# Kernel optimization log

Hardware: AMD Instinct MI355X
Metric: run time of the kernel (lower is better)

Reference implementation:

```python
import jax, jax.numpy as jnp
import numpy as np
from jax import lax

B = 4096
E = 8
D = 9216       # model_dim = 64*12*12
H = 128        # hidden_size_per_expert
O = 10         # output_dim


def setup_inputs() -> dict:
    key = jax.random.key(0)
    ks = jax.random.split(key, 10)
    s = lambda *sh: 1.0 / np.sqrt(np.prod(sh[1:]) if len(sh) > 1 else sh[0])
    return {
        "x": jax.random.normal(ks[0], (B, 1, 28, 28), jnp.float32),
        "conv1_w": jax.random.normal(ks[1], (32, 1, 3, 3), jnp.float32) * s(32, 1, 3, 3),
        "conv1_b": jnp.zeros((32,), jnp.float32),
        "conv2_w": jax.random.normal(ks[2], (64, 32, 3, 3), jnp.float32) * s(64, 32, 3, 3),
        "conv2_b": jnp.zeros((64,), jnp.float32),
        "gate_w": jax.random.normal(ks[3], (D, E), jnp.float32) * s(D, E),
        "w1": jax.random.normal(ks[4], (E, D, H), jnp.float32) * s(E, D, H),
        "b1": jnp.zeros((E, H), jnp.float32),
        "w2": jax.random.normal(ks[5], (E, H, O), jnp.float32) * s(E, H, O),
        "b2": jnp.zeros((E, O), jnp.float32),
    }


def _conv(x, w, b):
    y = lax.conv_general_dilated(x, w, (1, 1), "VALID",
                                 dimension_numbers=("NCHW", "OIHW", "NCHW"))
    return y + b[None, :, None, None]


def _maxpool2(x):
    return lax.reduce_window(x, -jnp.inf, lax.max,
                             (1, 1, 2, 2), (1, 1, 2, 2), "VALID")


def reference(x, conv1_w, conv1_b, conv2_w, conv2_b, gate_w, w1, b1, w2, b2):
    h = jax.nn.relu(_conv(x, conv1_w, conv1_b))            # [B,32,26,26]
    h = jax.nn.relu(_conv(h, conv2_w, conv2_b))            # [B,64,24,24]
    h = _maxpool2(h)                                       # [B,64,12,12]
    h = h.reshape(h.shape[0], -1)                          # [B,D]

    # top-1 gate: softmax over expert logits, pick argmax, scale by its prob
    logits = h @ gate_w                                    # [B,E]
    gates = jax.nn.softmax(logits, axis=-1)
    idx = jnp.argmax(logits, axis=-1)                      # [B]
    scale = jnp.take_along_axis(gates, idx[:, None], axis=1)  # [B,1]

    # expert FFN (computed densely per expert, selected per token)
    he = jax.nn.relu(jnp.einsum("bd,edh->beh", h, w1) + b1)   # [B,E,H]
    oe = jnp.einsum("beh,eho->beo", he, w2) + b2              # [B,E,O]
    out = jnp.take_along_axis(oe, idx[:, None, None], axis=1)[:, 0]  # [B,O]
    out = scale * out
    return jax.nn.log_softmax(out, axis=-1)
```

## Files before the change

kernel.cpp:

```cpp
#include <hip/hip_runtime.h>
#include <math.h>

namespace {
constexpr int kB = 4096;
constexpr int kD = 9216;
constexpr int kE = 8;
constexpr int kH = 128;
constexpr int kO = 10;
constexpr int PSTR = 32;
constexpr int KSPLIT = 8;

typedef __attribute__((ext_vector_type(8))) short short8;
typedef __attribute__((ext_vector_type(4))) float f32x4;
typedef __attribute__((ext_vector_type(4))) unsigned u32x4;

__device__ inline unsigned f2bf(float f) {
  unsigned u = __float_as_uint(f);
  return (u + 0x7fffu + ((u >> 16) & 1u)) >> 16;
}
__device__ inline float bf2f(unsigned b) { return __uint_as_float(b << 16); }

__device__ inline unsigned cvtpk(float a, float b) {
  unsigned d;
  asm("v_cvt_pk_bf16_f32 %0, %1, %2" : "=v"(d) : "v"(a), "v"(b));
  return d;
}
__device__ inline void hilo_pair(float a, float b, unsigned& hp, unsigned& lp) {
  hp = cvtpk(a, b);
  float ra = a - __uint_as_float(hp << 16);
  float rb = b - __uint_as_float(hp & 0xffff0000u);
  lp = cvtpk(ra, rb);
}

__global__ __launch_bounds__(256) void prep_w1(
    const float* __restrict__ w1, ushort* __restrict__ w1ph,
    ushort* __restrict__ w1pl, const float* __restrict__ c2w,
    ushort* __restrict__ Bph, ushort* __restrict__ Bpl,
    int* __restrict__ counts) {
  if (blockIdx.x == 0) {
    if (threadIdx.x < kE) counts[threadIdx.x] = 0;
    for (int i = threadIdx.x; i < 9 * 4 * 64 * 8; i += 256) {
      int j = i & 7, lane = (i >> 3) & 63, nt = (i >> 9) & 3, tap = i >> 11;
      int n = nt * 16 + (lane & 15);
      int c1 = (lane >> 4) * 8 + j;
      float v = c2w[(n * 32 + c1) * 9 + tap];
      unsigned hb = f2bf(v);
      Bph[i] = (ushort)hb;
      Bpl[i] = (ushort)f2bf(v - bf2f(hb));
    }
  }
  int t = blockIdx.x * 256 + threadIdx.x;
  int n = t & 127;
  int rem = t >> 7;
  int k8 = rem % 1152;
  int e = rem / 1152;
  const float* src = w1 + ((size_t)e * kD + (size_t)k8 * 8) * kH + n;
  float v[8];
#pragma unroll
  for (int j = 0; j < 8; ++j) v[j] = src[(size_t)j * kH];
  u32x4 hw, lw;
#pragma unroll
  for (int j = 0; j < 4; ++j) {
    unsigned hp, lp;
    hilo_pair(v[2 * j], v[2 * j + 1], hp, lp);
    hw[j] = hp;
    lw[j] = lp;
  }
  size_t base =
      ((((size_t)e * 288 + (k8 >> 2)) * 8 + (n >> 4)) * 64 +
       (((k8 & 3) << 4) | (n & 15))) * 8;
  *(u32x4*)(w1ph + base) = hw;
  *(u32x4*)(w1pl + base) = lw;
}

__global__ __launch_bounds__(256, 2) void conv_kernel(
    const float* __restrict__ x, const float* __restrict__ c1w,
    const float* __restrict__ c1b, const float* __restrict__ b2g,
    const ushort* __restrict__ Bph, const ushort* __restrict__ Bpl,
    float* __restrict__ h) {
  __shared__ float xs[784];
  __shared__ float w1s[288];
  __shared__ float b1s[32];
  __shared__ ushort h1h[364 * PSTR];
  __shared__ ushort h1l[364 * PSTR];
  const int b = blockIdx.x, tid = threadIdx.x;
  const int lane = tid & 63, wave = tid >> 6;

  short8 Bh[9], Bl[9];
#pragma unroll
  for (int tap = 0; tap < 9; ++tap) {
    int fi = ((tap * 4 + wave) * 64 + lane) * 8;
    Bh[tap] = *(const short8*)(Bph + fi);
    Bl[tap] = *(const short8*)(Bpl + fi);
  }
  float b2v = b2g[wave * 16 + (lane & 15)];

  const float* xb = x + (size_t)b * 784;
  for (int i = tid; i < 784; i += 256) xs[i] = xb[i];
  for (int i = tid; i < 288; i += 256) w1s[i] = c1w[i];
  if (tid < 32) b1s[tid] = c1b[tid];
  __syncthreads();

  float* hb = h + (size_t)b * kD;
  for (int pass = 0; pass < 2; ++pass) {
    for (int i = tid; i < 364 * 16; i += 256) {
      int p = i >> 4, cp = (i & 15) * 2;
      int r = p / 26, col = p - r * 26;
      const float* xr = xs + (pass * 12 + r) * 28 + col;
      const float* w0 = w1s + cp * 9;
      float v0 = b1s[cp], v1 = b1s[cp + 1];
#pragma unroll
      for (int ky = 0; ky < 3; ++ky)
#pragma unroll
        for (int kx = 0; kx < 3; ++kx) {
          float xv = xr[ky * 28 + kx];
          v0 += xv * w0[ky * 3 + kx];
          v1 += xv * w0[9 + ky * 3 + kx];
        }
      v0 = fmaxf(v0, 0.f);
      v1 = fmaxf(v1, 0.f);
      unsigned hp, lp;
      hilo_pair(v0, v1, hp, lp);
      *(unsigned*)&h1h[p * PSTR + cp] = hp;
      *(unsigned*)&h1l[p * PSTR + cp] = lp;
    }
    __syncthreads();
    const int m = lane & 15, kg = lane >> 4;
    for (int mt = 0; mt < 18; ++mt) {
      int cell = mt * 4 + (m >> 2), sub = m & 3;
      int cy = cell / 12, cx = cell - cy * 12;
      int yy = 2 * cy + (sub >> 1), xx = 2 * cx + (sub & 1);
      const ushort* ah = h1h + (yy * 26 + xx) * PSTR + kg * 8;
      const ushort* al = h1l + (yy * 26 + xx) * PSTR + kg * 8;
      f32x4 acc = {0.f, 0.f, 0.f, 0.f};
#pragma unroll
      for (int ky = 0; ky < 3; ++ky)
#pragma unroll
        for (int kx = 0; kx < 3; ++kx) {
          const int tap = ky * 3 + kx;
          short8 Ah = *(const short8*)(ah + (ky * 26 + kx) * PSTR);
          short8 Al = *(const short8*)(al + (ky * 26 + kx) * PSTR);
          acc = __builtin_amdgcn_mfma_f32_16x16x32_bf16(Al, Bh[tap], acc, 0, 0, 0);
          acc = __builtin_amdgcn_mfma_f32_16x16x32_bf16(Ah, Bl[tap], acc, 0, 0, 0);
          acc = __builtin_amdgcn_mfma_f32_16x16x32_bf16(Ah, Bh[tap], acc, 0, 0, 0);
        }
      int cellg = mt * 4 + kg;
      int gy = cellg / 12, gx = cellg - gy * 12;
      int orow = (pass * 6 + gy) * 12 + gx;
      float p0 = fmaxf(fmaxf(acc[0], acc[1]), fmaxf(acc[2], acc[3]));
      hb[(wave * 16 + m) * 144 + orow] = fmaxf(p0 + b2v, 0.f);
    }
    __syncthreads();
  }
}

__global__ __launch_bounds__(256) void gate_kernel(
    const float* __restrict__ h, const float* __restrict__ gw,
    int* __restrict__ idx, float* __restrict__ scale,
    int* __restrict__ counts) {
  const int b = blockIdx.x * 4 + (threadIdx.x >> 6);
  const int lane = threadIdx.x & 63;
  const float* hb = h + (size_t)b * kD;
  float acc[kE] = {0, 0, 0, 0, 0, 0, 0, 0};
  for (int i = lane; i < kD; i += 64) {
    float hv = hb[i];
    const float* g = gw + (size_t)i * kE;
#pragma unroll
    for (int e = 0; e < kE; ++e) acc[e] += hv * g[e];
  }
#pragma unroll
  for (int off = 32; off > 0; off >>= 1) {
#pragma unroll
    for (int e = 0; e < kE; ++e) acc[e] += __shfl_down(acc[e], off, 64);
  }
  if (lane == 0) {
    float m = acc[0];
    int bi = 0;
#pragma unroll
    for (int e = 1; e < kE; ++e)
      if (acc[e] > m) { m = acc[e]; bi = e; }
    float s = 0.f;
#pragma unroll
    for (int e = 0; e < kE; ++e) s += expf(acc[e] - m);
    idx[b] = bi;
    scale[b] = 1.0f / s;
    atomicAdd(&counts[bi], 1);
  }
}

__global__ __launch_bounds__(256) void scan_scatter(
    const int* __restrict__ counts, const int* __restrict__ idx,
    int* __restrict__ offsets, int* __restrict__ perm) {
  __shared__ int soff[kE + 1];
  __shared__ int cur[kE];
  if (threadIdx.x == 0) {
    int o = 0;
    for (int e = 0; e < kE; ++e) {
      soff[e] = o;
      cur[e] = o;
      o += counts[e];
    }
    soff[kE] = o;
  }
  __syncthreads();
  for (int b = threadIdx.x; b < kB; b += 256) {
    int e = idx[b];
    int pos = atomicAdd(&cur[e], 1);
    perm[pos] = b;
  }
  if (threadIdx.x <= kE) offsets[threadIdx.x] = soff[threadIdx.x];
}

__global__ __launch_bounds__(256) void expert_gemm(
    const float* __restrict__ h, const ushort* __restrict__ w1ph,
    const ushort* __restrict__ w1pl, const int* __restrict__ perm,
    const int* __restrict__ offsets, float* __restrict__ preact) {
  const int e = blockIdx.x, ks = blockIdx.y;
  const int start = offsets[e] + blockIdx.z * 64;
  const int end = offsets[e + 1];
  if (start >= end) return;
  const int M = min(64, end - start);
  __shared__ ushort Afh[4096];
  __shared__ ushort Afl[4096];
  __shared__ ushort Bsh[8192];
  __shared__ ushort Bsl[8192];
  __shared__ int rows[64];
  const int tid = threadIdx.x;
  if (tid < 64) rows[tid] = perm[start + min(tid, M - 1)];
  __syncthreads();
  const int wave = tid >> 6, lane = tid & 63;
  const int m15 = lane & 15, kg4 = lane >> 4;
  const int srow = tid >> 2, spart = tid & 3;
  const int kbase = ks * (kD / KSPLIT);
  const float* hp0 = h + (size_t)rows[srow] * kD + kbase + spart * 16;
  const int skstep = spart >> 1, skg = (spart & 1) * 2;
  const int sg = srow >> 4, sm = srow & 15;
  ushort* wh0 = &Afh[((skstep * 4 + sg) * 64 + skg * 16 + sm) * 8];
  ushort* wl0 = &Afl[((skstep * 4 + sg) * 64 + skg * 16 + sm) * 8];
  f32x4 acc[8];
#pragma unroll
  for (int j = 0; j < 8; ++j) acc[j] = {0.f, 0.f, 0.f, 0.f};

  for (int bk = 0; bk < kD / KSPLIT; bk += 64) {
#pragma unroll
    for (int c = 0; c < 2; ++c) {
      float4 v0 = *(const float4*)(hp0 + bk + c * 8);
      float4 v1 = *(const float4*)(hp0 + bk + c * 8 + 4);
      float f[8] = {v0.x, v0.y, v0.z, v0.w, v1.x, v1.y, v1.z, v1.w};
      u32x4 hw, lw;
#pragma unroll
      for (int j = 0; j < 4; ++j) {
        unsigned hp, lp;
        hilo_pair(f[2 * j], f[2 * j + 1], hp, lp);
        hw[j] = hp;
        lw[j] = lp;
      }
      *(u32x4*)(wh0 + c * 128) = hw;
      *(u32x4*)(wl0 + c * 128) = lw;
    }
    {
      const size_t bbase =
          ((size_t)e * 288 + ((kbase + bk) >> 5)) * 4096;
#pragma unroll
      for (int q = 0; q < 4; ++q) {
        int c = tid + q * 256;
        *(short8*)&Bsh[c * 8] = *(const short8*)(w1ph + bbase + (size_t)c * 8);
        *(short8*)&Bsl[c * 8] = *(const short8*)(w1pl + bbase + (size_t)c * 8);
      }
    }
    __syncthreads();
#pragma unroll
    for (int kstep = 0; kstep < 2; ++kstep) {
      const ushort* af = &Afh[((kstep * 4 + wave) * 64 + lane) * 8];
      short8 ah = *(const short8*)af;
      short8 al = *(const short8*)(af + (Afl - Afh));
      const ushort* bph = &Bsh[kstep * 4096 + lane * 8];
      const ushort* bpl = &Bsl[kstep * 4096 + lane * 8];
#pragma unroll
      for (int nt = 0; nt < 8; ++nt) {
        short8 bh = *(const short8*)(bph + nt * 512);
        short8 bl = *(const short8*)(bpl + nt * 512);
        acc[nt] = __builtin_amdgcn_mfma_f32_16x16x32_bf16(al, bh, acc[nt], 0, 0, 0);
        acc[nt] = __builtin_amdgcn_mfma_f32_16x16x32_bf16(ah, bl, acc[nt], 0, 0, 0);
        acc[nt] = __builtin_amdgcn_mfma_f32_16x16x32_bf16(ah, bh, acc[nt], 0, 0, 0);
      }
    }
    __syncthreads();
  }
  float* pb = preact + (size_t)ks * kB * kH;
#pragma unroll
  for (int r = 0; r < 4; ++r) {
    int row = wave * 16 + kg4 * 4 + r;
    if (row < M) {
      float* pr = pb + (size_t)rows[row] * kH + m15;
#pragma unroll
      for (int nt = 0; nt < 8; ++nt) pr[nt * 16] = acc[nt][r];
    }
  }
}

__global__ __launch_bounds__(64) void expert_tail(
    const float* __restrict__ preact, const float* __restrict__ b1,
    const float* __restrict__ w2, const float* __restrict__ b2,
    const int* __restrict__ idx, const float* __restrict__ scale,
    float* __restrict__ out) {
  const int b = blockIdx.x;
  const int lane = threadIdx.x;
  const int e = idx[b];
  float pa = 0.f, pc = 0.f;
#pragma unroll
  for (int ks = 0; ks < KSPLIT; ++ks) {
    const float* ps = preact + ((size_t)ks * kB + b) * kH;
    pa += ps[lane];
    pc += ps[64 + lane];
  }
  float hea = fmaxf(pa + b1[e * kH + lane], 0.f);
  float heb = fmaxf(pc + b1[e * kH + 64 + lane], 0.f);
  const float* w2a = w2 + ((size_t)e * kH + lane) * kO;
  const float* w2b = w2a + 64 * kO;
  float part[kO];
#pragma unroll
  for (int o = 0; o < kO; ++o) part[o] = hea * w2a[o] + heb * w2b[o];
#pragma unroll
  for (int off = 32; off > 0; off >>= 1)
#pragma unroll
    for (int o = 0; o < kO; ++o) part[o] += __shfl_down(part[o], off, 64);
  if (lane == 0) {
    const float sc = scale[b];
    float v[kO], m = -1e30f;
#pragma unroll
    for (int o = 0; o < kO; ++o) {
      v[o] = (part[o] + b2[e * kO + o]) * sc;
      m = fmaxf(m, v[o]);
    }
    float s = 0.f;
#pragma unroll
    for (int o = 0; o < kO; ++o) s += expf(v[o] - m);
    const float lse = m + logf(s);
#pragma unroll
    for (int o = 0; o < kO; ++o) out[(size_t)b * kO + o] = v[o] - lse;
  }
}

}

extern "C" void kernel_launch(void* const* d_in, const int* in_sizes, int n_in,
                              void* d_out, int out_size, void* d_ws,
                              size_t ws_size, hipStream_t stream) {
  (void)in_sizes; (void)n_in; (void)out_size; (void)ws_size;
  const float* x   = (const float*)d_in[0];
  const float* c1w = (const float*)d_in[1];
  const float* c1b = (const float*)d_in[2];
  const float* c2w = (const float*)d_in[3];
  const float* c2b = (const float*)d_in[4];
  const float* gw  = (const float*)d_in[5];
  const float* w1  = (const float*)d_in[6];
  const float* b1  = (const float*)d_in[7];
  const float* w2  = (const float*)d_in[8];
  const float* b2  = (const float*)d_in[9];
  float* out = (float*)d_out;

  char* ws = (char*)d_ws;
  float* h = (float*)ws;
  size_t off = (size_t)kB * kD * sizeof(float);
  ushort* w1ph = (ushort*)(ws + off); off += (size_t)kE * kD * kH * 2;
  ushort* w1pl = (ushort*)(ws + off); off += (size_t)kE * kD * kH * 2;
  float* preact = (float*)(ws + off); off += (size_t)KSPLIT * kB * kH * 4;
  ushort* Bph = (ushort*)(ws + off);  off += 9 * 4 * 64 * 8 * 2;
  ushort* Bpl = (ushort*)(ws + off);  off += 9 * 4 * 64 * 8 * 2;
  int* idx = (int*)(ws + off);        off += (size_t)kB * 4;
  float* scale = (float*)(ws + off);  off += (size_t)kB * 4;
  int* perm = (int*)(ws + off);       off += (size_t)kB * 4;
  int* counts = (int*)(ws + off);     off += 64;
  int* offsets = (int*)(ws + off);    off += 64;

  prep_w1<<<4608, 256, 0, stream>>>(w1, w1ph, w1pl, c2w, Bph, Bpl, counts);
  conv_kernel<<<kB, 256, 0, stream>>>(x, c1w, c1b, c2b, Bph, Bpl, h);
  gate_kernel<<<kB / 4, 256, 0, stream>>>(h, gw, idx, scale, counts);
  scan_scatter<<<1, 256, 0, stream>>>(counts, idx, offsets, perm);
  dim3 eg(kE, KSPLIT, 16);
  expert_gemm<<<eg, 256, 0, stream>>>(h, w1ph, w1pl, perm, offsets, preact);
  expert_tail<<<kB, 64, 0, stream>>>(preact, b1, w2, b2, idx, scale, out);
}
```

Baseline: 541.0 us.

## Retile conv2 MFMA so each wave covers 2 channel tiles and half the rows

Conv2 work is redistributed so each wave handles two 16-channel output tiles over nine of the eighteen row tiles, instead of one channel tile over all eighteen. Each A fragment loaded from LDS is now reused across two B tiles, which halves LDS A reads. B fragments are reloaded from global memory in groups of three taps rather than kept resident for all nine taps. Launch bounds are raised to three blocks per CU to allow more occupancy, at the cost of 18 live accumulators per wave and repeated global B loads per pass.

```diff
diff --git a/kernel.cpp b/kernel.cpp
--- a/kernel.cpp
+++ b/kernel.cpp
@@ -73,7 +73,7 @@
   *(u32x4*)(w1pl + base) = lw;
 }
 
-__global__ __launch_bounds__(256, 2) void conv_kernel(
+__global__ __launch_bounds__(256, 3) void conv_kernel(
     const float* __restrict__ x, const float* __restrict__ c1w,
     const float* __restrict__ c1b, const float* __restrict__ b2g,
     const ushort* __restrict__ Bph, const ushort* __restrict__ Bpl,
@@ -85,15 +85,13 @@
   __shared__ ushort h1l[364 * PSTR];
   const int b = blockIdx.x, tid = threadIdx.x;
   const int lane = tid & 63, wave = tid >> 6;
-
-  short8 Bh[9], Bl[9];
-#pragma unroll
-  for (int tap = 0; tap < 9; ++tap) {
-    int fi = ((tap * 4 + wave) * 64 + lane) * 8;
-    Bh[tap] = *(const short8*)(Bph + fi);
-    Bl[tap] = *(const short8*)(Bpl + fi);
-  }
-  float b2v = b2g[wave * 16 + (lane & 15)];
+  const int n0 = (wave & 1) * 2;
+  const int mtb = (wave >> 1) * 9;
+  const int m = lane & 15, kg = lane >> 4;
+
+  float b2v[2];
+  b2v[0] = b2g[n0 * 16 + m];
+  b2v[1] = b2g[(n0 + 1) * 16 + m];
 
   const float* xb = x + (size_t)b * 784;
   for (int i = tid; i < 784; i += 256) xs[i] = xb[i];
@@ -125,30 +123,63 @@
       *(unsigned*)&h1l[p * PSTR + cp] = lp;
     }
     __syncthreads();
-    const int m = lane & 15, kg = lane >> 4;
-    for (int mt = 0; mt < 18; ++mt) {
+
+    int pbase[9];
+#pragma unroll
+    for (int i = 0; i < 9; ++i) {
+      int mt = mtb + i;
       int cell = mt * 4 + (m >> 2), sub = m & 3;
       int cy = cell / 12, cx = cell - cy * 12;
       int yy = 2 * cy + (sub >> 1), xx = 2 * cx + (sub & 1);
-      const ushort* ah = h1h + (yy * 26 + xx) * PSTR + kg * 8;
-      const ushort* al = h1l + (yy * 26 + xx) * PSTR + kg * 8;
-      f32x4 acc = {0.f, 0.f, 0.f, 0.f};
-#pragma unroll
-      for (int ky = 0; ky < 3; ++ky)
-#pragma unroll
-        for (int kx = 0; kx < 3; ++kx) {
-          const int tap = ky * 3 + kx;
-          short8 Ah = *(const short8*)(ah + (ky * 26 + kx) * PSTR);
-          short8 Al = *(const short8*)(al + (ky * 26 + kx) * PSTR);
-          acc = __builtin_amdgcn_mfma_f32_16x16x32_bf16(Al, Bh[tap], acc, 0, 0, 0);
-          acc = __builtin_amdgcn_mfma_f32_16x16x32_bf16(Ah, Bl[tap], acc, 0, 0, 0);
-          acc = __builtin_amdgcn_mfma_f32_16x16x32_bf16(Ah, Bh[tap], acc, 0, 0, 0);
+      pbase[i] = (yy * 26 + xx) * PSTR + kg * 8;
+    }
+    f32x4 acc[9][2];
+#pragma unroll
+    for (int i = 0; i < 9; ++i) {
+      acc[i][0] = {0.f, 0.f, 0.f, 0.f};
+      acc[i][1] = {0.f, 0.f, 0.f, 0.f};
+    }
+#pragma unroll
+    for (int g = 0; g < 3; ++g) {
+      short8 Bh[3][2], Bl[3][2];
+#pragma unroll
+      for (int t = 0; t < 3; ++t)
+#pragma unroll
+        for (int nt = 0; nt < 2; ++nt) {
+          int fi = (((3 * g + t) * 4 + n0 + nt) * 64 + lane) * 8;
+          Bh[t][nt] = *(const short8*)(Bph + fi);
+          Bl[t][nt] = *(const short8*)(Bpl + fi);
         }
+#pragma unroll
+      for (int i = 0; i < 9; ++i) {
+#pragma unroll
+        for (int t = 0; t < 3; ++t) {
+          const int tap = 3 * g + t;
+          const int ky = tap / 3, kx = tap - ky * 3;
+          const int toff = (ky * 26 + kx) * PSTR;
+          short8 Ah = *(const short8*)(h1h + pbase[i] + toff);
+          short8 Al = *(const short8*)(h1l + pbase[i] + toff);
+          acc[i][0] = __builtin_amdgcn_mfma_f32_16x16x32_bf16(Al, Bh[t][0], acc[i][0], 0, 0, 0);
+          acc[i][0] = __builtin_amdgcn_mfma_f32_16x16x32_bf16(Ah, Bl[t][0], acc[i][0], 0, 0, 0);
+          acc[i][0] = __builtin_amdgcn_mfma_f32_16x16x32_bf16(Ah, Bh[t][0], acc[i][0], 0, 0, 0);
+          acc[i][1] = __builtin_amdgcn_mfma_f32_16x16x32_bf16(Al, Bh[t][1], acc[i][1], 0, 0, 0);
+          acc[i][1] = __builtin_amdgcn_mfma_f32_16x16x32_bf16(Ah, Bl[t][1], acc[i][1], 0, 0, 0);
+          acc[i][1] = __builtin_amdgcn_mfma_f32_16x16x32_bf16(Ah, Bh[t][1], acc[i][1], 0, 0, 0);
+        }
+      }
+    }
+#pragma unroll
+    for (int i = 0; i < 9; ++i) {
+      int mt = mtb + i;
       int cellg = mt * 4 + kg;
       int gy = cellg / 12, gx = cellg - gy * 12;
       int orow = (pass * 6 + gy) * 12 + gx;
-      float p0 = fmaxf(fmaxf(acc[0], acc[1]), fmaxf(acc[2], acc[3]));
-      hb[(wave * 16 + m) * 144 + orow] = fmaxf(p0 + b2v, 0.f);
+#pragma unroll
+      for (int nt = 0; nt < 2; ++nt) {
+        float p0 = fmaxf(fmaxf(acc[i][nt][0], acc[i][nt][1]),
+                         fmaxf(acc[i][nt][2], acc[i][nt][3]));
+        hb[((n0 + nt) * 16 + m) * 144 + orow] = fmaxf(p0 + b2v[nt], 0.f);
+      }
     }
     __syncthreads();
   }
```

Measured after the change: 689.4 us. 27.4% more time.
